# Kernel optimization log

Measured on AMD Instinct MI355X. Metric: run time of the kernel, lower is better.

Reference implementation:

```python
import jax, jax.numpy as jnp
import numpy as np

N, IN_DIM, HID, HEADS, OUT_DIM = 50000, 128, 64, 2, 40
E = 1_600_000
NEG_SLOPE = 0.2


def _glorot(key, shape):
    fan_in, fan_out = shape[0], shape[-1]
    lim = float(np.sqrt(6.0 / (fan_in + fan_out)))
    return jax.random.uniform(key, shape, jnp.float32, -lim, lim)


def setup_inputs() -> dict:
    key = jax.random.key(0)
    ks = jax.random.split(key, 20)
    x = jax.random.normal(ks[0], (N, IN_DIM), jnp.float32)
    edge_index = jax.random.randint(ks[1], (2, E), 0, N, jnp.int32)
    d = {"x": x, "edge_index": edge_index}
    # GAT layer 0: in=IN_DIM, out=HEADS*HID
    d["Wl0"] = _glorot(ks[2], (IN_DIM, HEADS * HID))
    d["bl0"] = jnp.zeros((HEADS * HID,), jnp.float32)
    d["Wr0"] = _glorot(ks[3], (IN_DIM, HEADS * HID))
    d["br0"] = jnp.zeros((HEADS * HID,), jnp.float32)
    d["al0"] = _glorot(ks[4], (HEADS, HID))
    d["ar0"] = _glorot(ks[5], (HEADS, HID))
    # GAT layer 1: in=HEADS*HID
    d["Wl1"] = _glorot(ks[6], (HEADS * HID, HEADS * HID))
    d["bl1"] = jnp.zeros((HEADS * HID,), jnp.float32)
    d["Wr1"] = _glorot(ks[7], (HEADS * HID, HEADS * HID))
    d["br1"] = jnp.zeros((HEADS * HID,), jnp.float32)
    d["al1"] = _glorot(ks[8], (HEADS, HID))
    d["ar1"] = _glorot(ks[9], (HEADS, HID))
    # post_mp: Linear(HEADS*HID, HID) -> Linear(HID, OUT_DIM)
    d["Wm1"] = _glorot(ks[10], (HEADS * HID, HID))
    d["bm1"] = jnp.zeros((HID,), jnp.float32)
    d["Wm2"] = _glorot(ks[11], (HID, OUT_DIM))
    d["bm2"] = jnp.zeros((OUT_DIM,), jnp.float32)
    return d


def _gat_layer(x, Wl, bl, Wr, br, al, ar, src, dst):
    # x: [N, F_in] -> [N, HEADS*HID]
    xl = (x @ Wl + bl).reshape(N, HEADS, HID)
    xr = (x @ Wr + br).reshape(N, HEADS, HID)
    alpha_l = jnp.einsum('nhc,hc->nh', xl, al)  # [N,H]
    alpha_r = jnp.einsum('nhc,hc->nh', xr, ar)  # [N,H]
    # per-edge attention logits: alpha_j (src) + alpha_i (dst)
    e = jax.nn.leaky_relu(alpha_l[src] + alpha_r[dst], NEG_SLOPE)  # [E,H]
    # segment softmax over incoming edges of each dst node
    m = jax.ops.segment_max(e, dst, num_segments=N)
    ex = jnp.exp(e - m[dst])
    s = jax.ops.segment_sum(ex, dst, num_segments=N)
    a = ex / (s[dst] + 1e-16)  # [E,H]
    # weighted scatter-sum of source features
    out = jax.ops.segment_sum(xl[src] * a[:, :, None], dst, num_segments=N)  # [N,H,C]
    return out.reshape(N, HEADS * HID)


def reference(x, edge_index, Wl0, bl0, Wr0, br0, al0, ar0,
              Wl1, bl1, Wr1, br1, al1, ar1, Wm1, bm1, Wm2, bm2):
    src, dst = edge_index[0], edge_index[1]
    h = jax.nn.relu(_gat_layer(x, Wl0, bl0, Wr0, br0, al0, ar0, src, dst))
    h = jax.nn.relu(_gat_layer(h, Wl1, bl1, Wr1, br1, al1, ar1, src, dst))
    h = (h @ Wm1 + bm1) @ Wm2 + bm2  # post_mp (dropout p=0.0)
    return jax.nn.log_softmax(h, axis=1)
```

## Files before the change

### kernel.cpp

```cpp
#include <hip/hip_runtime.h>
#include <hip/hip_fp16.h>
#include <math.h>

#define NN   50000
#define EE   1600000
#define FD   128
#define OUTD 40
#define NEG  0.2f
#define NB   196
#define ABLK 256
#define ACH  (EE/ABLK)
#define SLOTB 80
#define BMAX 9216
#define BPSZ (9*4*64*8)
#define SETUP_BLOCKS 2304

__device__ __forceinline__ float lrelu(float v) { return v > 0.f ? v : NEG * v; }

__device__ __forceinline__ int fenc(float f) { int b = __float_as_int(f); return b < 0 ? (b ^ 0x7FFFFFFF) : b; }
__device__ __forceinline__ float fdec(int v) { v = v < 0 ? (v ^ 0x7FFFFFFF) : v; return __int_as_float(v); }

__device__ __forceinline__ unsigned short f2bf(float f) {
  unsigned int u = __float_as_uint(f);
  unsigned int r = u + 0x7FFFu + ((u >> 16) & 1u);
  return (unsigned short)(r >> 16);
}

typedef short bf16x8 __attribute__((ext_vector_type(8)));
typedef float f32x4  __attribute__((ext_vector_type(4)));

__global__ __launch_bounds__(256) void k_setup(
    const float* __restrict__ X,
    const int* __restrict__ srcE, const int* __restrict__ dstE,
    const float* __restrict__ Wl0, const float* __restrict__ Wr0, const float* __restrict__ ar0,
    const float* __restrict__ br0,
    const float* __restrict__ Wl1, const float* __restrict__ Wr1, const float* __restrict__ ar1,
    const float* __restrict__ br1,
    const float* __restrict__ Wm1, const float* __restrict__ bm1,
    const float* __restrict__ Wm2, const float* __restrict__ bm2,
    unsigned short* __restrict__ XB,
    unsigned short* __restrict__ Bp0, unsigned short* __restrict__ Bp1,
    float* __restrict__ brd0, float* __restrict__ brd1,
    float* __restrict__ Wp, float* __restrict__ bp,
    int* __restrict__ mAL,
    int* __restrict__ cnt, unsigned int* __restrict__ pslot)
{
  __shared__ int lcur[NB];
  int t = threadIdx.x;
  int bid = blockIdx.x;
  if (bid < 256) {
    if (t < NB) lcur[t] = 0;
    __syncthreads();
    int e0 = bid * ACH;
    size_t base = (size_t)bid * NB * SLOTB;
    for (int e = e0 + t; e < e0 + ACH; e += 256) {
      int d = dstE[e];
      int b = d >> 8;
      int p = atomicAdd(&lcur[b], 1);
      pslot[base + (size_t)b*SLOTB + p] = (unsigned int)srcE[e] | ((unsigned int)(d & 255) << 16);
    }
    __syncthreads();
    if (t < NB) cnt[bid*NB + t] = lcur[t];
  } else if (bid < 264) {
    int rb = bid - 256;
    for (int i = rb*256 + t; i < FD*OUTD; i += 8*256) {
      int k = i / OUTD, o = i % OUTD;
      float s = 0.f;
      for (int j = 0; j < 64; ++j) s += Wm1[k*64 + j] * Wm2[j*OUTD + o];
      Wp[i] = s;
    }
  } else if (bid == 264) {
    if (t < OUTD) {
      float s = bm2[t];
      for (int j = 0; j < 64; ++j) s += bm1[j] * Wm2[j*OUTD + t];
      bp[t] = s;
    }
    if (t >= 64 && t < 68) {
      int idx = t - 64, l = idx >> 1, h = idx & 1;
      const float* br = l ? br1 : br0;
      const float* ar = l ? ar1 : ar0;
      float s = 0.f;
      for (int c = 0; c < 64; ++c) s += br[h*64 + c] * ar[h*64 + c];
      (l ? brd1 : brd0)[h] = s;
    }
    if (t >= 96 && t < 100) mAL[t - 96] = 0x80000000;
  } else if (bid >= 272 && bid < 416) {
    bool l1 = (bid >= 344);
    const float* Wl = l1 ? Wl1 : Wl0;
    const float* Wr = l1 ? Wr1 : Wr0;
    const float* ar = l1 ? ar1 : ar0;
    unsigned short* Bp = l1 ? Bp1 : Bp0;
    int i = (bid - (l1 ? 344 : 272))*256 + t;
    if (i < BPSZ) {
      int j = i & 7, lane = (i >> 3) & 63, ks = (i >> 9) & 3, ct = i >> 11;
      int k = ks*32 + 8*(lane >> 4) + j;
      int c = lane & 15;
      float v = 0.f;
      if (ct < 8) v = Wl[k*FD + ct*16 + c];
      else if (c < 2) {
        for (int c2 = 0; c2 < 64; ++c2) v += Wr[k*FD + c*64 + c2] * ar[c*64 + c2];
      }
      Bp[i] = f2bf(v);
    }
  } else if (bid >= 416) {
    const int n4 = NN*FD/4;
    for (int i = (bid-416)*256 + t; i < n4; i += (gridDim.x-416)*256) {
      float4 v = ((const float4*)X)[i];
      ushort4 o;
      o.x = f2bf(v.x); o.y = f2bf(v.y); o.z = f2bf(v.z); o.w = f2bf(v.w);
      ((ushort4*)XB)[i] = o;
    }
  }
}

#define SMEM_BYTES 59392
__global__ __launch_bounds__(256) void k_bfgemm(
    const unsigned int* __restrict__ pslot, const int* __restrict__ cnt,
    int* __restrict__ row_off, unsigned short* __restrict__ csr16,
    const unsigned short* __restrict__ XB, const unsigned short* __restrict__ Bp,
    const float* __restrict__ bl, const float* __restrict__ al, const float* __restrict__ brd,
    __half* __restrict__ XLh, float* __restrict__ AL, float* __restrict__ AR,
    int* __restrict__ mAL)
{
  __shared__ char smem[SMEM_BYTES];
  int t = threadIdx.x;
  int bid = blockIdx.x;
  if (bid < NB) {
    int* scnt = (int*)smem;
    int* soff = (int*)(smem + 1024);
    unsigned int* pairs = (unsigned int*)(smem + 2048);
    unsigned short* stage = (unsigned short*)(smem + 38912);
    int* hist = (int*)(smem + 57344);
    int* rel  = (int*)(smem + 58368);
    int g = bid;
    int v = cnt[t*NB + g];
    scnt[t] = v;
    soff[t] = v;
    __syncthreads();
    #pragma unroll
    for (int off = 1; off < 256; off <<= 1) {
      int u = (t >= off) ? soff[t - off] : 0;
      __syncthreads();
      soff[t] += u;
      __syncthreads();
    }
    int cnt_g = soff[255];
    int mybase = soff[t] - v;
    {
      const unsigned int* sp = pslot + (size_t)t * NB * SLOTB + (size_t)g * SLOTB;
      for (int i = 0; i < v; ++i) pairs[mybase + i] = sp[i];
    }
    __syncthreads();
    hist[t] = 0;
    __syncthreads();
    for (int i = t; i < cnt_g; i += 256)
      atomicAdd(&hist[pairs[i] >> 16], 1);
    __syncthreads();
    int hv = hist[t];
    rel[t] = hv;
    __syncthreads();
    #pragma unroll
    for (int off = 1; off < 256; off <<= 1) {
      int u = (t >= off) ? rel[t - off] : 0;
      __syncthreads();
      rel[t] += u;
      __syncthreads();
    }
    int excl = rel[t] - hv;
    __syncthreads();
    rel[t] = excl;
    row_off[g*257 + t] = g*BMAX + excl;
    if (t == 0) row_off[g*257 + 256] = g*BMAX + cnt_g;
    hist[t] = 0;
    __syncthreads();
    for (int i = t; i < cnt_g; i += 256) {
      unsigned int p = pairs[i];
      int j = p >> 16;
      int l = atomicAdd(&hist[j], 1);
      stage[rel[j] + l] = (unsigned short)(p & 0xFFFF);
    }
    __syncthreads();
    size_t cbase = (size_t)g * BMAX;
    for (int i = t; i < cnt_g; i += 256) csr16[cbase + i] = stage[i];
  } else {
    unsigned short* sB = (unsigned short*)smem;
    int* smaxI = (int*)(smem + 36864);
    if (t < 2) smaxI[t] = 0x80000000;
    {
      const uint4* s = (const uint4*)Bp;
      uint4* d = (uint4*)sB;
      #pragma unroll
      for (int i = 0; i < 9; ++i) d[t + i*256] = s[t + i*256];
    }
    __syncthreads();
    int w = t >> 6, l = t & 63;
    int c = l & 15, kg = l >> 4;
    int rowbase = (bid - NB)*64 + w*16;
    int arow = rowbase + c; if (arow > NN-1) arow = NN-1;
    f32x4 acc[9] = {};
    const bf16x8* sBf = (const bf16x8*)sB;
    #pragma unroll
    for (int ks = 0; ks < 4; ++ks) {
      bf16x8 afrag = *(const bf16x8*)(XB + (size_t)arow*FD + ks*32 + kg*8);
      #pragma unroll
      for (int ct = 0; ct < 9; ++ct)
        acc[ct] = __builtin_amdgcn_mfma_f32_16x16x32_bf16(afrag, sBf[(ct*4+ks)*64 + l], acc[ct], 0, 0, 0);
    }
    float pAL0[4] = {}, pAL1[4] = {};
    #pragma unroll
    for (int ct = 0; ct < 8; ++ct) {
      float bias = bl[ct*16 + c];
      float alv  = al[ct*16 + c];
      #pragma unroll
      for (int r = 0; r < 4; ++r) {
        int row = rowbase + kg*4 + r;
        float xv = acc[ct][r] + bias;
        if (row < NN) XLh[(size_t)row*FD + ct*16 + c] = __float2half(xv);
        if (ct < 4) pAL0[r] = fmaf(xv, alv, pAL0[r]);
        else        pAL1[r] = fmaf(xv, alv, pAL1[r]);
      }
    }
    if (c < 2) {
      float b = brd[c];
      #pragma unroll
      for (int r = 0; r < 4; ++r) {
        int row = rowbase + kg*4 + r;
        if (row < NN) AR[(size_t)row*2 + c] = acc[8][r] + b;
      }
    }
    float m0 = -INFINITY, m1 = -INFINITY;
    #pragma unroll
    for (int r = 0; r < 4; ++r) {
      float v0 = pAL0[r], v1 = pAL1[r];
      #pragma unroll
      for (int off = 1; off < 16; off <<= 1) { v0 += __shfl_xor(v0, off); v1 += __shfl_xor(v1, off); }
      int row = rowbase + kg*4 + r;
      if (c == 0 && row < NN) {
        AL[(size_t)row*2 + 0] = v0;
        AL[(size_t)row*2 + 1] = v1;
        m0 = fmaxf(m0, v0); m1 = fmaxf(m1, v1);
      }
    }
    if (c == 0) { atomicMax(&smaxI[0], fenc(m0)); atomicMax(&smaxI[1], fenc(m1)); }
    __syncthreads();
    if (t < 2) atomicMax(&mAL[t], smaxI[t]);
  }
}

__global__ __launch_bounds__(256) void k_gemm_mfma(
    const unsigned short* __restrict__ XB, const unsigned short* __restrict__ Bp,
    const float* __restrict__ bl, const float* __restrict__ al, const float* __restrict__ brd,
    __half* __restrict__ XLh, float* __restrict__ AL, float* __restrict__ AR,
    int* __restrict__ mAL)
{
  __shared__ unsigned short sB[BPSZ];
  __shared__ int smaxI[2];
  int t = threadIdx.x;
  if (t < 2) smaxI[t] = 0x80000000;
  {
    const uint4* s = (const uint4*)Bp;
    uint4* d = (uint4*)sB;
    #pragma unroll
    for (int i = 0; i < 9; ++i) d[t + i*256] = s[t + i*256];
  }
  __syncthreads();
  int w = t >> 6, l = t & 63;
  int c = l & 15, kg = l >> 4;
  int rowbase = blockIdx.x*64 + w*16;
  int arow = rowbase + c; if (arow > NN-1) arow = NN-1;
  f32x4 acc[9] = {};
  const bf16x8* sBf = (const bf16x8*)sB;
  #pragma unroll
  for (int ks = 0; ks < 4; ++ks) {
    bf16x8 afrag = *(const bf16x8*)(XB + (size_t)arow*FD + ks*32 + kg*8);
    #pragma unroll
    for (int ct = 0; ct < 9; ++ct)
      acc[ct] = __builtin_amdgcn_mfma_f32_16x16x32_bf16(afrag, sBf[(ct*4+ks)*64 + l], acc[ct], 0, 0, 0);
  }
  float pAL0[4] = {}, pAL1[4] = {};
  #pragma unroll
  for (int ct = 0; ct < 8; ++ct) {
    float bias = bl[ct*16 + c];
    float alv  = al[ct*16 + c];
    #pragma unroll
    for (int r = 0; r < 4; ++r) {
      int row = rowbase + kg*4 + r;
      float xv = acc[ct][r] + bias;
      if (row < NN) XLh[(size_t)row*FD + ct*16 + c] = __float2half(xv);
      if (ct < 4) pAL0[r] = fmaf(xv, alv, pAL0[r]);
      else        pAL1[r] = fmaf(xv, alv, pAL1[r]);
    }
  }
  if (c < 2) {
    float b = brd[c];
    #pragma unroll
    for (int r = 0; r < 4; ++r) {
      int row = rowbase + kg*4 + r;
      if (row < NN) AR[(size_t)row*2 + c] = acc[8][r] + b;
    }
  }
  float m0 = -INFINITY, m1 = -INFINITY;
  #pragma unroll
  for (int r = 0; r < 4; ++r) {
    float v0 = pAL0[r], v1 = pAL1[r];
    #pragma unroll
    for (int off = 1; off < 16; off <<= 1) { v0 += __shfl_xor(v0, off); v1 += __shfl_xor(v1, off); }
    int row = rowbase + kg*4 + r;
    if (c == 0 && row < NN) {
      AL[(size_t)row*2 + 0] = v0;
      AL[(size_t)row*2 + 1] = v1;
      m0 = fmaxf(m0, v0); m1 = fmaxf(m1, v1);
    }
  }
  if (c == 0) { atomicMax(&smaxI[0], fenc(m0)); atomicMax(&smaxI[1], fenc(m1)); }
  __syncthreads();
  if (t < 2) atomicMax(&mAL[t], smaxI[t]);
}

template<bool BF16OUT>
__global__ __launch_bounds__(256) void k_agg(
    const __half* __restrict__ XLh, const float* __restrict__ AL,
    const float* __restrict__ AR, const int* __restrict__ mAL,
    const int* __restrict__ row_off, const unsigned short* __restrict__ csr16,
    float* __restrict__ OUTf, unsigned short* __restrict__ OUTb)
{
  int node = blockIdx.x * 4 + (threadIdx.x >> 6);
  if (node >= NN) return;
  int lane = threadIdx.x & 63;
  int g = lane >> 4, l = lane & 15;
  bool h1 = (l & 8) != 0;
  float2 ar = ((const float2*)AR)[node];
  float m0 = lrelu(fdec(mAL[0]) + ar.x);
  float m1 = lrelu(fdec(mAL[1]) + ar.y);
  float ar_s = h1 ? ar.y : ar.x;
  float m_s  = h1 ? m1 : m0;
  int ro = node + (node >> 8);
  int beg = row_off[ro], end = row_off[ro + 1];
  float facc[8] = {};
  __half2 hacc[4];
  #pragma unroll
  for (int q = 0; q < 4; ++q) hacc[q] = __half2half2(__float2half(0.f));
  float s_acc = 0.f;
  int flushcnt = 0;
  if (beg < end) {
    int em1 = end - 1;
    int s0 = csr16[min(beg + g,      em1)];
    int s1 = csr16[min(beg + 4 + g,  em1)];
    int s2 = csr16[min(beg + 8 + g,  em1)];
    int s3 = csr16[min(beg + 12 + g, em1)];
    for (int i = beg; i < end; i += 16) {
      int c0 = s0, c1 = s1, c2 = s2, c3 = s3;
      bool v0 = (i + g) < end, v1 = (i + 4 + g) < end,
           v2 = (i + 8 + g) < end, v3 = (i + 12 + g) < end;
      int ni = i + 16;
      if (ni < end) {
        s0 = csr16[min(ni + g,      em1)];
        s1 = csr16[min(ni + 4 + g,  em1)];
        s2 = csr16[min(ni + 8 + g,  em1)];
        s3 = csr16[min(ni + 12 + g, em1)];
      }
      uint4 d0 = *(const uint4*)(XLh + (size_t)c0*FD + 8*l);
      uint4 d1 = *(const uint4*)(XLh + (size_t)c1*FD + 8*l);
      uint4 d2 = *(const uint4*)(XLh + (size_t)c2*FD + 8*l);
      uint4 d3 = *(const uint4*)(XLh + (size_t)c3*FD + 8*l);
      float2 a0 = ((const float2*)AL)[c0];
      float2 a1 = ((const float2*)AL)[c1];
      float2 a2 = ((const float2*)AL)[c2];
      float2 a3 = ((const float2*)AL)[c3];
      float w0 = __expf(lrelu((h1 ? a0.y : a0.x) + ar_s) - m_s);
      float w1 = __expf(lrelu((h1 ? a1.y : a1.x) + ar_s) - m_s);
      float w2 = __expf(lrelu((h1 ? a2.y : a2.x) + ar_s) - m_s);
      float w3 = __expf(lrelu((h1 ? a3.y : a3.x) + ar_s) - m_s);
      w0 = v0 ? w0 : 0.f; w1 = v1 ? w1 : 0.f;
      w2 = v2 ? w2 : 0.f; w3 = v3 ? w3 : 0.f;
      s_acc += (w0 + w1) + (w2 + w3);
      __half2 h0 = __half2half2(__float2half(w0));
      __half2 h1w = __half2half2(__float2half(w1));
      __half2 h2 = __half2half2(__float2half(w2));
      __half2 h3 = __half2half2(__float2half(w3));
      const __half2* f0 = (const __half2*)&d0;
      const __half2* f1 = (const __half2*)&d1;
      const __half2* f2 = (const __half2*)&d2;
      const __half2* f3 = (const __half2*)&d3;
      #pragma unroll
      for (int q = 0; q < 4; ++q) {
        hacc[q] = __hfma2(h0,  f0[q], hacc[q]);
        hacc[q] = __hfma2(h1w, f1[q], hacc[q]);
        hacc[q] = __hfma2(h2,  f2[q], hacc[q]);
        hacc[q] = __hfma2(h3,  f3[q], hacc[q]);
      }
      if (++flushcnt == 8) {
        flushcnt = 0;
        #pragma unroll
        for (int q = 0; q < 4; ++q) {
          float2 f = __half22float2(hacc[q]);
          facc[2*q] += f.x; facc[2*q+1] += f.y;
          hacc[q] = __half2half2(__float2half(0.f));
        }
      }
    }
    #pragma unroll
    for (int q = 0; q < 4; ++q) {
      float2 f = __half22float2(hacc[q]);
      facc[2*q] += f.x; facc[2*q+1] += f.y;
    }
  }
  #pragma unroll
  for (int off = 16; off < 64; off <<= 1) {
    s_acc += __shfl_xor(s_acc, off);
    #pragma unroll
    for (int q = 0; q < 8; ++q) facc[q] += __shfl_xor(facc[q], off);
  }
  if (g == 0) {
    float sinv = 1.f / (s_acc + 1e-16f);
    float o[8];
    #pragma unroll
    for (int q = 0; q < 8; ++q) o[q] = fmaxf(facc[q]*sinv, 0.f);
    if constexpr (BF16OUT) {
      unsigned short ob[8];
      #pragma unroll
      for (int q = 0; q < 8; ++q) ob[q] = f2bf(o[q]);
      *(uint4*)&OUTb[(size_t)node*FD + 8*l] = *(uint4*)ob;
    } else {
      float4 o0, o1;
      o0.x = o[0]; o0.y = o[1]; o0.z = o[2]; o0.w = o[3];
      o1.x = o[4]; o1.y = o[5]; o1.z = o[6]; o1.w = o[7];
      *(float4*)&OUTf[(size_t)node*FD + 8*l]     = o0;
      *(float4*)&OUTf[(size_t)node*FD + 8*l + 4] = o1;
    }
  }
}

__global__ __launch_bounds__(256) void k_post(
    const float* __restrict__ H, const float* __restrict__ Wp, const float* __restrict__ bp,
    float* __restrict__ out)
{
  __shared__ float sW[FD*OUTD];
  __shared__ float sB[OUTD];
  __shared__ float sX[64][FD+1];
  int t = threadIdx.x;
  for (int i = t; i < FD*OUTD; i += 256) sW[i] = Wp[i];
  if (t < OUTD) sB[t] = bp[t];
  int base = blockIdx.x * 64;
  int rows = NN - base; if (rows > 64) rows = 64;
  const float4* H4 = (const float4*)(H + (size_t)base * FD);
  int nf4 = rows * (FD/4);
  for (int i = t; i < nf4; i += 256) {
    float4 v = H4[i];
    int n = i >> 5, c = (i & 31) * 4;
    sX[n][c] = v.x; sX[n][c+1] = v.y; sX[n][c+2] = v.z; sX[n][c+3] = v.w;
  }
  __syncthreads();
  int n = t >> 2, cg = t & 3;
  int node = base + n;
  float acc[10];
  #pragma unroll
  for (int j = 0; j < 10; ++j) acc[j] = sB[cg*10 + j];
  #pragma unroll 4
  for (int k = 0; k < FD; ++k) {
    float xv = sX[n][k];
    const float* wrow = &sW[k*OUTD + cg*10];
    #pragma unroll
    for (int j = 0; j < 10; ++j) acc[j] = fmaf(xv, wrow[j], acc[j]);
  }
  float m = acc[0];
  #pragma unroll
  for (int j = 1; j < 10; ++j) m = fmaxf(m, acc[j]);
  m = fmaxf(m, __shfl_xor(m, 1));
  m = fmaxf(m, __shfl_xor(m, 2));
  float s = 0.f;
  #pragma unroll
  for (int j = 0; j < 10; ++j) s += __expf(acc[j] - m);
  s += __shfl_xor(s, 1);
  s += __shfl_xor(s, 2);
  float lg = m + __logf(s);
  if (node < NN) {
    #pragma unroll
    for (int j = 0; j < 10; ++j) out[(size_t)node*OUTD + cg*10 + j] = acc[j] - lg;
  }
}

extern "C" void kernel_launch(void* const* d_in, const int* in_sizes, int n_in,
                              void* d_out, int out_size, void* d_ws, size_t ws_size,
                              hipStream_t stream)
{
  const float* x   = (const float*)d_in[0];
  const int*   ei  = (const int*)d_in[1];
  const float* Wl0 = (const float*)d_in[2];
  const float* bl0 = (const float*)d_in[3];
  const float* Wr0 = (const float*)d_in[4];
  const float* br0 = (const float*)d_in[5];
  const float* al0 = (const float*)d_in[6];
  const float* ar0 = (const float*)d_in[7];
  const float* Wl1 = (const float*)d_in[8];
  const float* bl1 = (const float*)d_in[9];
  const float* Wr1 = (const float*)d_in[10];
  const float* br1 = (const float*)d_in[11];
  const float* al1 = (const float*)d_in[12];
  const float* ar1 = (const float*)d_in[13];
  const float* Wm1 = (const float*)d_in[14];
  const float* bm1 = (const float*)d_in[15];
  const float* Wm2 = (const float*)d_in[16];
  const float* bm2 = (const float*)d_in[17];
  const int* srcA = ei;
  const int* dstA = ei + EE;

  char* w = (char*)d_ws;
  __half* XLh    = (__half*)w;          w += (size_t)NN*FD*2;
  float* bufB    = (float*)w;           w += (size_t)NN*FD*4;
  unsigned short* XB = (unsigned short*)w; w += (size_t)NN*FD*2;
  float* AL      = (float*)w;  w += (size_t)NN*2*4;
  float* AR      = (float*)w;  w += (size_t)NN*2*4;
  float* brd0    = (float*)w;  w += 16;
  float* brd1    = (float*)w;  w += 16;
  float* Wp      = (float*)w;  w += FD*OUTD*4;
  float* bp      = (float*)w;  w += 64*4;
  int* mAL       = (int*)w;    w += 4*4;
  int* row_off   = (int*)w;    w += (size_t)(NB*257 + 1)*4 + 12;
  unsigned short* csr16 = (unsigned short*)w; w += (size_t)NB*BMAX*2;
  unsigned short* Bp0   = (unsigned short*)w; w += BPSZ*2;
  unsigned short* Bp1   = (unsigned short*)w; w += BPSZ*2;
  unsigned int* pslot = (unsigned int*)bufB;
  int* cnt = (int*)((char*)bufB + (size_t)ABLK*NB*SLOTB*4);

  k_setup<<<SETUP_BLOCKS, 256, 0, stream>>>(x, srcA, dstA,
                                            Wl0, Wr0, ar0, br0, Wl1, Wr1, ar1, br1,
                                            Wm1, bm1, Wm2, bm2, XB, Bp0, Bp1,
                                            brd0, brd1, Wp, bp, mAL, cnt, pslot);

  k_bfgemm<<<NB + (NN+63)/64, 256, 0, stream>>>(pslot, cnt, row_off, csr16,
                                                XB, Bp0, bl0, al0, brd0, XLh, AL, AR, mAL + 0);
  k_agg<true><<<(NN+3)/4, 256, 0, stream>>>(XLh, AL, AR, mAL + 0, row_off, csr16, nullptr, XB);
  k_gemm_mfma<<<(NN+63)/64, 256, 0, stream>>>(XB, Bp1, bl1, al1, brd1, XLh, AL, AR, mAL + 2);
  k_agg<false><<<(NN+3)/4, 256, 0, stream>>>(XLh, AL, AR, mAL + 2, row_off, csr16, bufB, nullptr);
  k_post<<<(NN+63)/64, 256, 0, stream>>>(bufB, Wp, bp, (float*)d_out);
}
```

Before: 190.2 us.

## Fuse post-MLP projection and log-softmax into second aggregation kernel

The final linear projection and log_softmax move into the epilogue of the layer-1 aggregation kernel, which removes the separate k_post launch and the fp32 round trip of the hidden features through global memory. Each aggregation block now loads the 128x40 projection weights into shared memory (about 20 KB). With 4 nodes per block, that means 12500 blocks each repeating the weight load. The per-node matvec is split across the 4 lane groups with cross-lane shuffle reductions, and the early return for out-of-range nodes is removed (NN is divisible by 4).

Measured after the change: 369.7 us. 1.94x slower.

```diff
diff --git a/kernel.cpp b/kernel.cpp
--- a/kernel.cpp
+++ b/kernel.cpp
@@ -14,6 +14,7 @@
 #define BMAX 9216
 #define BPSZ (9*4*64*8)
 #define SETUP_BLOCKS 2304
+#define POST_SMEM (FD*OUTD*4 + 64*4)
 
 __device__ __forceinline__ float lrelu(float v) { return v > 0.f ? v : NEG * v; }
 
@@ -322,11 +323,20 @@
     const __half* __restrict__ XLh, const float* __restrict__ AL,
     const float* __restrict__ AR, const int* __restrict__ mAL,
     const int* __restrict__ row_off, const unsigned short* __restrict__ csr16,
-    float* __restrict__ OUTf, unsigned short* __restrict__ OUTb)
+    const float* __restrict__ Wp, const float* __restrict__ bp,
+    float* __restrict__ out, unsigned short* __restrict__ OUTb)
 {
-  int node = blockIdx.x * 4 + (threadIdx.x >> 6);
-  if (node >= NN) return;
-  int lane = threadIdx.x & 63;
+  extern __shared__ char dynsmem[];
+  float* sWp = (float*)dynsmem;
+  float* sbp = sWp + FD*OUTD;
+  int t = threadIdx.x;
+  if constexpr (!BF16OUT) {
+    for (int i = t; i < FD*OUTD; i += 256) sWp[i] = Wp[i];
+    if (t < OUTD) sbp[t] = bp[t];
+    __syncthreads();
+  }
+  int node = blockIdx.x * 4 + (t >> 6);
+  int lane = t & 63;
   int g = lane >> 4, l = lane & 15;
   bool h1 = (l & 8) != 0;
   float2 ar = ((const float2*)AR)[node];
@@ -411,72 +421,52 @@
     #pragma unroll
     for (int q = 0; q < 8; ++q) facc[q] += __shfl_xor(facc[q], off);
   }
-  if (g == 0) {
-    float sinv = 1.f / (s_acc + 1e-16f);
-    float o[8];
-    #pragma unroll
-    for (int q = 0; q < 8; ++q) o[q] = fmaxf(facc[q]*sinv, 0.f);
-    if constexpr (BF16OUT) {
+  float sinv = 1.f / (s_acc + 1e-16f);
+  float o[8];
+  #pragma unroll
+  for (int q = 0; q < 8; ++q) o[q] = fmaxf(facc[q]*sinv, 0.f);
+  if constexpr (BF16OUT) {
+    if (g == 0) {
       unsigned short ob[8];
       #pragma unroll
       for (int q = 0; q < 8; ++q) ob[q] = f2bf(o[q]);
       *(uint4*)&OUTb[(size_t)node*FD + 8*l] = *(uint4*)ob;
-    } else {
-      float4 o0, o1;
-      o0.x = o[0]; o0.y = o[1]; o0.z = o[2]; o0.w = o[3];
-      o1.x = o[4]; o1.y = o[5]; o1.z = o[6]; o1.w = o[7];
-      *(float4*)&OUTf[(size_t)node*FD + 8*l]     = o0;
-      *(float4*)&OUTf[(size_t)node*FD + 8*l + 4] = o1;
-    }
-  }
-}
-
-__global__ __launch_bounds__(256) void k_post(
-    const float* __restrict__ H, const float* __restrict__ Wp, const float* __restrict__ bp,
-    float* __restrict__ out)
-{
-  __shared__ float sW[FD*OUTD];
-  __shared__ float sB[OUTD];
-  __shared__ float sX[64][FD+1];
-  int t = threadIdx.x;
-  for (int i = t; i < FD*OUTD; i += 256) sW[i] = Wp[i];
-  if (t < OUTD) sB[t] = bp[t];
-  int base = blockIdx.x * 64;
-  int rows = NN - base; if (rows > 64) rows = 64;
-  const float4* H4 = (const float4*)(H + (size_t)base * FD);
-  int nf4 = rows * (FD/4);
-  for (int i = t; i < nf4; i += 256) {
-    float4 v = H4[i];
-    int n = i >> 5, c = (i & 31) * 4;
-    sX[n][c] = v.x; sX[n][c+1] = v.y; sX[n][c+2] = v.z; sX[n][c+3] = v.w;
-  }
-  __syncthreads();
-  int n = t >> 2, cg = t & 3;
-  int node = base + n;
-  float acc[10];
-  #pragma unroll
-  for (int j = 0; j < 10; ++j) acc[j] = sB[cg*10 + j];
-  #pragma unroll 4
-  for (int k = 0; k < FD; ++k) {
-    float xv = sX[n][k];
-    const float* wrow = &sW[k*OUTD + cg*10];
-    #pragma unroll
-    for (int j = 0; j < 10; ++j) acc[j] = fmaf(xv, wrow[j], acc[j]);
-  }
-  float m = acc[0];
-  #pragma unroll
-  for (int j = 1; j < 10; ++j) m = fmaxf(m, acc[j]);
-  m = fmaxf(m, __shfl_xor(m, 1));
-  m = fmaxf(m, __shfl_xor(m, 2));
-  float s = 0.f;
-  #pragma unroll
-  for (int j = 0; j < 10; ++j) s += __expf(acc[j] - m);
-  s += __shfl_xor(s, 1);
-  s += __shfl_xor(s, 2);
-  float lg = m + __logf(s);
-  if (node < NN) {
-    #pragma unroll
-    for (int j = 0; j < 10; ++j) out[(size_t)node*OUTD + cg*10 + j] = acc[j] - lg;
+    }
+  } else {
+    int myo = 10 * g;
+    float part[10];
+    #pragma unroll
+    for (int j = 0; j < 10; ++j) part[j] = 0.f;
+    #pragma unroll
+    for (int d = 0; d < 8; ++d) {
+      float hv = o[d];
+      const float* wrow = &sWp[(8*l + d)*OUTD + myo];
+      #pragma unroll
+      for (int j = 0; j < 10; ++j) part[j] = fmaf(hv, wrow[j], part[j]);
+    }
+    #pragma unroll
+    for (int off = 1; off < 16; off <<= 1) {
+      #pragma unroll
+      for (int j = 0; j < 10; ++j) part[j] += __shfl_xor(part[j], off);
+    }
+    float z[10];
+    #pragma unroll
+    for (int j = 0; j < 10; ++j) z[j] = part[j] + sbp[myo + j];
+    float mx = z[0];
+    #pragma unroll
+    for (int j = 1; j < 10; ++j) mx = fmaxf(mx, z[j]);
+    mx = fmaxf(mx, __shfl_xor(mx, 16));
+    mx = fmaxf(mx, __shfl_xor(mx, 32));
+    float se = 0.f;
+    #pragma unroll
+    for (int j = 0; j < 10; ++j) se += __expf(z[j] - mx);
+    se += __shfl_xor(se, 16);
+    se += __shfl_xor(se, 32);
+    float lg = mx + __logf(se);
+    if (l == 0) {
+      #pragma unroll
+      for (int j = 0; j < 10; ++j) out[(size_t)node*OUTD + myo + j] = z[j] - lg;
+    }
   }
 }
 
@@ -530,8 +520,9 @@
 
   k_bfgemm<<<NB + (NN+63)/64, 256, 0, stream>>>(pslot, cnt, row_off, csr16,
                                                 XB, Bp0, bl0, al0, brd0, XLh, AL, AR, mAL + 0);
-  k_agg<true><<<(NN+3)/4, 256, 0, stream>>>(XLh, AL, AR, mAL + 0, row_off, csr16, nullptr, XB);
+  k_agg<true><<<(NN+3)/4, 256, 0, stream>>>(XLh, AL, AR, mAL + 0, row_off, csr16,
+                                            nullptr, nullptr, nullptr, XB);
   k_gemm_mfma<<<(NN+63)/64, 256, 0, stream>>>(XB, Bp1, bl1, al1, brd1, XLh, AL, AR, mAL + 2);
-  k_agg<false><<<(NN+3)/4, 256, 0, stream>>>(XLh, AL, AR, mAL + 2, row_off, csr16, bufB, nullptr);
-  k_post<<<(NN+63)/64, 256, 0, stream>>>(bufB, Wp, bp, (float*)d_out);
+  k_agg<false><<<(NN+3)/4, 256, POST_SMEM, stream>>>(XLh, AL, AR, mAL + 2, row_off, csr16,
+                                                     Wp, bp, (float*)d_out, nullptr);
 }
```
